# Kernel tuning notes

Hardware: AMD Instinct MI355X
Metric: run time of the kernel (lower is better)

The kernel has to match this reference:

```python
import jax, jax.numpy as jnp
import numpy as np

N_NODES = 50000
N_EDGES = 800000
NUM_FEAT = 256
HID = 64
N_CLS = 40
N_LAYERS = 2
EPS = 0.3  # residual scale from __init__ eps


def setup_inputs() -> dict:
    key = jax.random.key(0)
    ks = jax.random.split(key, 8)
    x = jax.random.normal(ks[0], (N_NODES, NUM_FEAT), dtype=jnp.float32)
    edge_index = jax.random.randint(ks[1], (2, N_EDGES), 0, N_NODES, dtype=jnp.int64)
    # xavier-normal-ish scaled weights
    W1 = jax.random.normal(ks[2], (HID, NUM_FEAT), dtype=jnp.float32) * (1.414 * (2.0 / (HID + NUM_FEAT)) ** 0.5)
    b1 = jnp.zeros((HID,), dtype=jnp.float32)
    W2 = jax.random.normal(ks[3], (N_CLS, HID), dtype=jnp.float32) * (1.414 * (2.0 / (N_CLS + HID)) ** 0.5)
    b2 = jnp.zeros((N_CLS,), dtype=jnp.float32)
    gate_w = jax.random.normal(ks[4], (N_LAYERS, 2 * HID), dtype=jnp.float32) * (1.414 * (2.0 / (2 * HID + 1)) ** 0.5)
    gate_b = jnp.zeros((N_LAYERS,), dtype=jnp.float32)
    return {"x": x, "edge_index": edge_index, "W1": W1, "b1": b1,
            "W2": W2, "b2": b2, "gate_w": gate_w, "gate_b": gate_b}


def _forward(x, edge_index, W1, b1, W2, b2, gate_w, gate_b):
    row, col = edge_index[0], edge_index[1]  # row = source, col = target (PyG convention)
    n = x.shape[0]
    ones_e = jnp.ones((edge_index.shape[1],), dtype=x.dtype)
    # degree(row) clamped to >=1, then d^{-1/2}
    deg = jnp.clip(jax.ops.segment_sum(ones_e, row, num_segments=n), 1.0)
    nd = deg ** -0.5  # [N]
    # mean-aggregation denominator: incoming-edge counts per target node
    cnt = jnp.clip(jax.ops.segment_sum(ones_e, col, num_segments=n), 1.0)

    # dense input projection (dropout is eval-mode no-op)
    h = jax.nn.relu(x @ W1.T + b1)  # [N, H]
    raw = h

    nd_edge = nd[row] * nd[col]  # [E]
    for l in range(N_LAYERS):
        hr = h[row]  # [E, H] gather (source)
        hc = h[col]  # [E, H] gather (target)
        # gate: Linear(concat([h[row], h[col]])) == h[row]@w_a + h[col]@w_b
        g = jnp.tanh(hr @ gate_w[l, :HID] + hc @ gate_w[l, HID:] + gate_b[l])  # [E]
        norm = g * nd_edge  # [E]
        msg = norm[:, None] * (hc + hr)  # x_i + x_j, [E, H]
        agg = jax.ops.segment_sum(msg, col, num_segments=n) / cnt[:, None]  # scatter-mean
        h = EPS * raw + agg

    logits = h @ W2.T + b2
    return jax.nn.log_softmax(logits, axis=1)


def reference(x, edge_index, W1, b1, W2, b2, gate_w, gate_b):
    return _forward(x, edge_index, W1, b1, W2, b2, gate_w, gate_b)
```

## Files before the change

### kernel.cpp

```cpp
#include <hip/hip_runtime.h>
#include <math.h>

#define N_NODES 50000
#define N_EDGES 800000
#define NFEAT 256
#define HID 64
#define NCLS 40
#define EPS_RES 0.3f
#define ROWSZ 68
#define SCAN_BLOCKS ((N_NODES + 255) / 256)
#define EB 32
#define CHUNK (N_EDGES / EB)
#define NR 4
#define RNG (N_NODES / NR)

typedef unsigned int uint;
typedef unsigned short ushort;

__device__ __forceinline__ float bflo(uint u) { return __uint_as_float(u << 16); }
__device__ __forceinline__ float bfhi(uint u) { return __uint_as_float(u & 0xFFFF0000u); }
__device__ __forceinline__ uint bf16rne(float f) {
    uint u = __float_as_uint(f);
    return (u + 0x7FFFu + ((u >> 16) & 1u)) >> 16;
}
__device__ __forceinline__ uint bf16rne2(float a, float b) {
    return bf16rne(a) | (bf16rne(b) << 16);
}

__global__ __launch_bounds__(256) void hist_kernel(const int* __restrict__ row,
                                                   const int* __restrict__ col,
                                                   int* __restrict__ degM,
                                                   int* __restrict__ cntM,
                                                   int* __restrict__ rank_local) {
    __shared__ int hist[RNG];
    int t = threadIdx.x;
    int chunk = blockIdx.x;
    int lo = blockIdx.y * RNG;
    int side = blockIdx.z;
    for (int j = t; j < RNG; j += 256) hist[j] = 0;
    __syncthreads();
    const int* idx = side ? col : row;
    int e0 = chunk * CHUNK;
    if (side == 0) {
        for (int base = 0; base < CHUNK; base += 1024) {
            int vb[4];
#pragma unroll
            for (int j = 0; j < 4; j++) {
                int i = base + j * 256 + t;
                vb[j] = (i < CHUNK) ? idx[e0 + i] : -1;
            }
#pragma unroll
            for (int j = 0; j < 4; j++) {
                uint v = (uint)(vb[j] - lo);
                if (v < RNG) atomicAdd(&hist[v], 1);
            }
        }
    } else {
        for (int base = 0; base < CHUNK; base += 1024) {
            int vb[4], ib[4];
#pragma unroll
            for (int j = 0; j < 4; j++) {
                int i = base + j * 256 + t;
                ib[j] = i;
                vb[j] = (i < CHUNK) ? idx[e0 + i] : -1;
            }
#pragma unroll
            for (int j = 0; j < 4; j++) {
                uint v = (uint)(vb[j] - lo);
                if (v < RNG) rank_local[e0 + ib[j]] = atomicAdd(&hist[v], 1);
            }
        }
    }
    __syncthreads();
    int* M = side ? cntM : degM;
    for (int j = t; j < RNG; j += 256) M[chunk * N_NODES + lo + j] = hist[j];
}

__device__ __forceinline__ int block_excl_scan_256(int v, int t, int* wsum) {
    int lane = t & 63, w = t >> 6;
    int sv = v;
#pragma unroll
    for (int d = 1; d < 64; d <<= 1) {
        int o = __shfl_up(sv, d);
        if (lane >= d) sv += o;
    }
    if (lane == 63) wsum[w] = sv;
    __syncthreads();
    int add = 0;
    for (int i = 0; i < w; i++) add += wsum[i];
    return sv + add - v;
}

__global__ void scan1_kernel(const int* __restrict__ degM, int* __restrict__ cntM,
                             int* __restrict__ off, int* __restrict__ bsum,
                             float* __restrict__ nd, float* __restrict__ invcnt) {
    __shared__ int wsum[4];
    int t = threadIdx.x;
    int idx = blockIdx.x * 256 + t;
    int v = 0;
    if (idx < N_NODES) {
        int sD = 0;
#pragma unroll
        for (int c = 0; c < EB; c++) sD += degM[c * N_NODES + idx];
        int run = 0;
#pragma unroll
        for (int c = 0; c < EB; c++) {
            int cv = cntM[c * N_NODES + idx];
            cntM[c * N_NODES + idx] = run;
            run += cv;
        }
        v = run;
        if (sD < 1) sD = 1;
        nd[idx] = rsqrtf((float)sD);
        int cc = run; if (cc < 1) cc = 1;
        invcnt[idx] = 1.0f / (float)cc;
    }
    int excl = block_excl_scan_256(v, t, wsum);
    if (idx < N_NODES) off[idx] = excl;
    if (t == 255) bsum[blockIdx.x] = excl + v;
}

__global__ void scan2_kernel(int* __restrict__ bsum) {
    __shared__ int wsum[4];
    int t = threadIdx.x;
    int v = (t < SCAN_BLOCKS) ? bsum[t] : 0;
    int excl = block_excl_scan_256(v, t, wsum);
    if (t < SCAN_BLOCKS) bsum[t] = excl;
}

__global__ void scan3_kernel(int* __restrict__ off, const int* __restrict__ bsum) {
    int t = threadIdx.x;
    int idx = blockIdx.x * 256 + t;
    if (idx < N_NODES) off[idx] += bsum[blockIdx.x];
    if (idx == 0) off[N_NODES] = N_EDGES;
}

__global__ void scatter_kernel(const int* __restrict__ row, const int* __restrict__ col,
                               const int* __restrict__ rank_local, const int* __restrict__ cntM,
                               const int* __restrict__ off, const float* __restrict__ nd,
                               int2* __restrict__ sedge) {
    int e = blockIdx.x * 256 + threadIdx.x;
    int r = row[e], c = col[e];
    int ch = e / CHUNK;
    int p = off[c] + cntM[ch * N_NODES + c] + rank_local[e];
    int2 se;
    se.x = r;
    se.y = __float_as_int(nd[r] * nd[c]);
    sedge[p] = se;
}

__global__ __launch_bounds__(256) void proj_kernel(const float* __restrict__ x,
                                                   const float* __restrict__ W1,
                                                   const float* __restrict__ b1,
                                                   const float* __restrict__ gw,
                                                   float* __restrict__ ha,
                                                   ushort* __restrict__ habf,
                                                   float* __restrict__ y,
                                                   float* __restrict__ z) {
    __shared__ float xs[64 * ROWSZ];
    __shared__ float ws[64 * ROWSZ];
    int t = threadIdx.x;
    int nb = blockIdx.x * 64;
    int lane = t & 63, w = t >> 6;
    int l15 = lane & 15, g = lane >> 4;
    int hbase = 16 * w + 4 * g;
    float acc[4][4];
#pragma unroll
    for (int j = 0; j < 4; j++)
#pragma unroll
        for (int i = 0; i < 4; i++) acc[j][i] = 0.f;

    for (int kc = 0; kc < NFEAT; kc += 64) {
        __syncthreads();
#pragma unroll
        for (int i = 0; i < 4; i++) {
            int idx = t + 256 * i;
            int r_ = idx >> 4;
            int kq = idx & 15;
            int gn = nb + r_;
            float4 v = make_float4(0.f, 0.f, 0.f, 0.f);
            if (gn < N_NODES) v = *(const float4*)(x + (size_t)gn * NFEAT + kc + kq * 4);
            *(float4*)(xs + r_ * ROWSZ + kq * 4) = v;
            float4 wv = *(const float4*)(W1 + (size_t)r_ * NFEAT + kc + kq * 4);
            *(float4*)(ws + r_ * ROWSZ + kq * 4) = wv;
        }
        __syncthreads();
#pragma unroll 4
        for (int k = 0; k < 64; k += 4) {
            float4 a[4], b[4];
#pragma unroll
            for (int j = 0; j < 4; j++) a[j] = *(const float4*)(xs + (l15 + 16 * j) * ROWSZ + k);
#pragma unroll
            for (int i = 0; i < 4; i++) b[i] = *(const float4*)(ws + (hbase + i) * ROWSZ + k);
#pragma unroll
            for (int j = 0; j < 4; j++)
#pragma unroll
                for (int i = 0; i < 4; i++)
                    acc[j][i] += a[j].x * b[i].x + a[j].y * b[i].y + a[j].z * b[i].z + a[j].w * b[i].w;
        }
    }
    float4 bias = *(const float4*)(b1 + hbase);
    float4 wa4 = *(const float4*)(gw + hbase);
    float4 wb4 = *(const float4*)(gw + HID + hbase);
    int slot = w * 4 + g;
    __syncthreads();
#pragma unroll
    for (int j = 0; j < 4; j++) {
        int gn = nb + l15 + 16 * j;
        float4 o;
        o.x = fmaxf(acc[j][0] + bias.x, 0.f);
        o.y = fmaxf(acc[j][1] + bias.y, 0.f);
        o.z = fmaxf(acc[j][2] + bias.z, 0.f);
        o.w = fmaxf(acc[j][3] + bias.w, 0.f);
        if (gn < N_NODES) {
            *(float4*)(ha + (size_t)gn * HID + hbase) = o;
            uint2 pk;
            pk.x = bf16rne2(o.x, o.y);
            pk.y = bf16rne2(o.z, o.w);
            *(uint2*)(habf + (size_t)gn * HID + hbase) = pk;
        }
        xs[(l15 + 16 * j) * 16 + slot] = o.x * wa4.x + o.y * wa4.y + o.z * wa4.z + o.w * wa4.w;
        ws[(l15 + 16 * j) * 16 + slot] = o.x * wb4.x + o.y * wb4.y + o.z * wb4.z + o.w * wb4.w;
    }
    __syncthreads();
    if (t < 64 && nb + t < N_NODES) {
        float sa = 0.f, sb = 0.f;
#pragma unroll
        for (int s = 0; s < 16; s++) { sa += xs[t * 16 + s]; sb += ws[t * 16 + s]; }
        y[nb + t] = sa;
        z[nb + t] = sb;
    }
}

__device__ __forceinline__ void agg_core8(const ushort* __restrict__ hbf,
                                          const int2* __restrict__ sedge,
                                          const float* __restrict__ y,
                                          float zc_b, int e0, int e1, int q, int c8,
                                          float acc[8], float& gs_out) {
#pragma unroll
    for (int i = 0; i < 8; i++) acc[i] = 0.f;
    float gs = 0.f;
    if (e0 < e1) {
        int eA = e0 + q;
        int ecA = (eA < e1) ? eA : e0;
        int2 seA = sedge[ecA];
        float ndeA = (eA < e1) ? __int_as_float(seA.y) : 0.f;
        int eB = e0 + 8 + q;
        int ecB = (eB < e1) ? eB : e0;
        int2 seB = sedge[ecB];
        float ndeB = (eB < e1) ? __int_as_float(seB.y) : 0.f;
        float yA = y[seA.x];
        uint4 uA = *(const uint4*)(hbf + (size_t)seA.x * HID + c8);
        for (int base = e0; base < e1; base += 8) {
            float yB = y[seB.x];
            uint4 uB = *(const uint4*)(hbf + (size_t)seB.x * HID + c8);
            int eC = base + 16 + q;
            int ecC = (eC < e1) ? eC : e0;
            int2 seC = sedge[ecC];
            float ndeC = (eC < e1) ? __int_as_float(seC.y) : 0.f;
            float gv = tanhf(yA + zc_b) * ndeA;
            acc[0] += gv * bflo(uA.x);
            acc[1] += gv * bfhi(uA.x);
            acc[2] += gv * bflo(uA.y);
            acc[3] += gv * bfhi(uA.y);
            acc[4] += gv * bflo(uA.z);
            acc[5] += gv * bfhi(uA.z);
            acc[6] += gv * bflo(uA.w);
            acc[7] += gv * bfhi(uA.w);
            gs += gv;
            yA = yB; uA = uB; ndeA = ndeB;
            seB = seC; ndeB = ndeC;
        }
    }
#pragma unroll
    for (int s = 8; s < 64; s <<= 1) {
#pragma unroll
        for (int i = 0; i < 8; i++) acc[i] += __shfl_xor(acc[i], s);
        gs += __shfl_xor(gs, s);
    }
    gs_out = gs;
}

__global__ void agg1_kernel(const float* __restrict__ ha, const ushort* __restrict__ habf,
                            const int2* __restrict__ sedge, const int* __restrict__ off,
                            const float* __restrict__ invcnt, const float* __restrict__ y,
                            const float* __restrict__ z, const float* __restrict__ gb,
                            const float* __restrict__ gw2, ushort* __restrict__ hbbf,
                            float* __restrict__ y2, float* __restrict__ z2) {
    int t = threadIdx.x;
    int lane = t & 63;
    int node = blockIdx.x * 4 + (t >> 6);
    int q = lane >> 3, c8 = (lane & 7) * 8;
    float4 ra = *(const float4*)(ha + (size_t)node * HID + c8);
    float4 rb = *(const float4*)(ha + (size_t)node * HID + c8 + 4);
    float raw8[8] = {ra.x, ra.y, ra.z, ra.w, rb.x, rb.y, rb.z, rb.w};
    float zc_b = z[node] + gb[0];
    float acc[8]; float gs;
    agg_core8(habf, sedge, y, zc_b, off[node], off[node + 1], q, c8, acc, gs);
    float invc = invcnt[node];
    float o[8];
#pragma unroll
    for (int i = 0; i < 8; i++) o[i] = EPS_RES * raw8[i] + (acc[i] + gs * raw8[i]) * invc;
    if (q == 0) {
        uint4 pk;
        pk.x = bf16rne2(o[0], o[1]);
        pk.y = bf16rne2(o[2], o[3]);
        pk.z = bf16rne2(o[4], o[5]);
        pk.w = bf16rne2(o[6], o[7]);
        *(uint4*)(hbbf + (size_t)node * HID + c8) = pk;
    }
    float4 wa0 = *(const float4*)(gw2 + c8);
    float4 wa1 = *(const float4*)(gw2 + c8 + 4);
    float4 wb0 = *(const float4*)(gw2 + HID + c8);
    float4 wb1 = *(const float4*)(gw2 + HID + c8 + 4);
    float p = o[0] * wa0.x + o[1] * wa0.y + o[2] * wa0.z + o[3] * wa0.w
            + o[4] * wa1.x + o[5] * wa1.y + o[6] * wa1.z + o[7] * wa1.w;
    float qq = o[0] * wb0.x + o[1] * wb0.y + o[2] * wb0.z + o[3] * wb0.w
             + o[4] * wb1.x + o[5] * wb1.y + o[6] * wb1.z + o[7] * wb1.w;
#pragma unroll
    for (int s = 1; s < 8; s <<= 1) { p += __shfl_xor(p, s); qq += __shfl_xor(qq, s); }
    if (lane == 0) { y2[node] = p; z2[node] = qq; }
}

__global__ void agg2_kernel(const ushort* __restrict__ hbbf, const float* __restrict__ ha,
                            const int2* __restrict__ sedge, const int* __restrict__ off,
                            const float* __restrict__ invcnt, const float* __restrict__ y2,
                            const float* __restrict__ z2, const float* __restrict__ gb,
                            const float* __restrict__ W2, const float* __restrict__ b2,
                            float* __restrict__ out) {
    __shared__ float w2s[NCLS * 65];
    __shared__ float b2s[NCLS];
    __shared__ float hs[4 * HID];
    int t = threadIdx.x;
    for (int i = t; i < NCLS * HID; i += 256) w2s[(i >> 6) * 65 + (i & 63)] = W2[i];
    if (t < NCLS) b2s[t] = b2[t];
    int lane = t & 63;
    int wv = t >> 6;
    int node = blockIdx.x * 4 + wv;
    int q = lane >> 3, c8 = (lane & 7) * 8;
    uint4 hc = *(const uint4*)(hbbf + (size_t)node * HID + c8);
    float hcv[8] = {bflo(hc.x), bfhi(hc.x), bflo(hc.y), bfhi(hc.y),
                    bflo(hc.z), bfhi(hc.z), bflo(hc.w), bfhi(hc.w)};
    float4 ra = *(const float4*)(ha + (size_t)node * HID + c8);
    float4 rb = *(const float4*)(ha + (size_t)node * HID + c8 + 4);
    float raw8[8] = {ra.x, ra.y, ra.z, ra.w, rb.x, rb.y, rb.z, rb.w};
    float zc_b = z2[node] + gb[0];
    float acc[8]; float gs;
    agg_core8(hbbf, sedge, y2, zc_b, off[node], off[node + 1], q, c8, acc, gs);
    float invc = invcnt[node];
    if (q == 0) {
        float4 o0, o1;
        o0.x = EPS_RES * raw8[0] + (acc[0] + gs * hcv[0]) * invc;
        o0.y = EPS_RES * raw8[1] + (acc[1] + gs * hcv[1]) * invc;
        o0.z = EPS_RES * raw8[2] + (acc[2] + gs * hcv[2]) * invc;
        o0.w = EPS_RES * raw8[3] + (acc[3] + gs * hcv[3]) * invc;
        o1.x = EPS_RES * raw8[4] + (acc[4] + gs * hcv[4]) * invc;
        o1.y = EPS_RES * raw8[5] + (acc[5] + gs * hcv[5]) * invc;
        o1.z = EPS_RES * raw8[6] + (acc[6] + gs * hcv[6]) * invc;
        o1.w = EPS_RES * raw8[7] + (acc[7] + gs * hcv[7]) * invc;
        *(float4*)(hs + wv * HID + c8) = o0;
        *(float4*)(hs + wv * HID + c8 + 4) = o1;
    }
    __syncthreads();
    float logit = 0.f;
    if (lane < NCLS) {
        const float* wr = w2s + lane * 65;
        const float* hrow = hs + wv * HID;
#pragma unroll
        for (int k = 0; k < HID; k++) logit += hrow[k] * wr[k];
        logit += b2s[lane];
    }
    float v = (lane < NCLS) ? logit : -INFINITY;
#pragma unroll
    for (int s = 1; s < 64; s <<= 1) v = fmaxf(v, __shfl_xor(v, s));
    float ex = (lane < NCLS) ? expf(logit - v) : 0.f;
#pragma unroll
    for (int s = 1; s < 64; s <<= 1) ex += __shfl_xor(ex, s);
    float ls = v + logf(ex);
    if (lane < NCLS) out[node * NCLS + lane] = logit - ls;
}

extern "C" void kernel_launch(void* const* d_in, const int* in_sizes, int n_in,
                              void* d_out, int out_size, void* d_ws, size_t ws_size,
                              hipStream_t stream) {
    const float* x  = (const float*)d_in[0];
    const int*   ei = (const int*)d_in[1];
    const float* W1 = (const float*)d_in[2];
    const float* b1 = (const float*)d_in[3];
    const float* W2 = (const float*)d_in[4];
    const float* b2 = (const float*)d_in[5];
    const float* gw = (const float*)d_in[6];
    const float* gb = (const float*)d_in[7];
    float* out = (float*)d_out;

    int2*  sedge  = (int2*)d_ws;
    float* nd     = (float*)(sedge + N_EDGES);
    float* invcnt = nd + N_NODES;
    float* y      = invcnt + N_NODES;
    float* z      = y + N_NODES;
    float* y2     = z + N_NODES;
    float* z2     = y2 + N_NODES;
    float* ha     = z2 + N_NODES;
    ushort* habf  = (ushort*)(ha + (size_t)N_NODES * HID);
    ushort* hbbf  = habf + (size_t)N_NODES * HID;
    int*   off    = (int*)(hbbf + (size_t)N_NODES * HID);
    int*   bsum   = off + N_NODES + 1;
    int*   degM   = (int*)ha;
    int*   cntM   = degM + (size_t)EB * N_NODES;
    int*   rank_local = (int*)habf;

    const int* row = ei;
    const int* col = ei + N_EDGES;

    hist_kernel<<<dim3(EB, NR, 2), 256, 0, stream>>>(row, col, degM, cntM, rank_local);
    scan1_kernel<<<SCAN_BLOCKS, 256, 0, stream>>>(degM, cntM, off, bsum, nd, invcnt);
    scan2_kernel<<<1, 256, 0, stream>>>(bsum);
    scan3_kernel<<<SCAN_BLOCKS, 256, 0, stream>>>(off, bsum);
    scatter_kernel<<<N_EDGES / 256, 256, 0, stream>>>(row, col, rank_local, cntM, off, nd, sedge);
    proj_kernel<<<(N_NODES + 63) / 64, 256, 0, stream>>>(x, W1, b1, gw, ha, habf, y, z);

    agg1_kernel<<<N_NODES / 4, 256, 0, stream>>>(ha, habf, sedge, off, invcnt, y, z, gb,
                                                 gw + 2 * HID, hbbf, y2, z2);
    agg2_kernel<<<N_NODES / 4, 256, 0, stream>>>(hbbf, ha, sedge, off, invcnt, y2, z2,
                                                 gb + 1, W2, b2, out);
}
```

Baseline: 268.1 us.

## Precompute per-edge gate weights in a separate kernel and drop the fp32 hidden copy

Adds a gate_kernel that computes tanh(y[src]+z[dst]+b) times the edge norm once per sorted edge. The scatter kernel now also writes a sorted target-column array for it to use. This removes the redundant per-lane tanh and y-gather from the aggregation inner loop, which now reads only a precomputed float per edge. The fp32 residual copy of h is also removed: both aggregation kernels read the residual from the bf16 buffer, which lowers precision. The cost is two extra edge-wide kernel launches and the writes and reads of an extra per-edge gate array.

Measured after the change: 285.0 us. 1.06x slower.

```diff
diff --git a/kernel.cpp b/kernel.cpp
--- a/kernel.cpp
+++ b/kernel.cpp
@@ -138,7 +138,7 @@
 __global__ void scatter_kernel(const int* __restrict__ row, const int* __restrict__ col,
                                const int* __restrict__ rank_local, const int* __restrict__ cntM,
                                const int* __restrict__ off, const float* __restrict__ nd,
-                               int2* __restrict__ sedge) {
+                               int2* __restrict__ sedge, int* __restrict__ scol) {
     int e = blockIdx.x * 256 + threadIdx.x;
     int r = row[e], c = col[e];
     int ch = e / CHUNK;
@@ -147,13 +147,13 @@
     se.x = r;
     se.y = __float_as_int(nd[r] * nd[c]);
     sedge[p] = se;
+    scol[p] = c;
 }
 
 __global__ __launch_bounds__(256) void proj_kernel(const float* __restrict__ x,
                                                    const float* __restrict__ W1,
                                                    const float* __restrict__ b1,
                                                    const float* __restrict__ gw,
-                                                   float* __restrict__ ha,
                                                    ushort* __restrict__ habf,
                                                    float* __restrict__ y,
                                                    float* __restrict__ z) {
@@ -213,7 +213,6 @@
         o.z = fmaxf(acc[j][2] + bias.z, 0.f);
         o.w = fmaxf(acc[j][3] + bias.w, 0.f);
         if (gn < N_NODES) {
-            *(float4*)(ha + (size_t)gn * HID + hbase) = o;
             uint2 pk;
             pk.x = bf16rne2(o.x, o.y);
             pk.y = bf16rne2(o.z, o.w);
@@ -232,10 +231,19 @@
     }
 }
 
+__global__ void gate_kernel(const int2* __restrict__ sedge, const int* __restrict__ scol,
+                            const float* __restrict__ y, const float* __restrict__ z,
+                            const float* __restrict__ gb, float* __restrict__ gnde) {
+    int e = blockIdx.x * 256 + threadIdx.x;
+    int2 se = sedge[e];
+    float g = tanhf(y[se.x] + z[scol[e]] + gb[0]);
+    gnde[e] = g * __int_as_float(se.y);
+}
+
 __device__ __forceinline__ void agg_core8(const ushort* __restrict__ hbf,
                                           const int2* __restrict__ sedge,
-                                          const float* __restrict__ y,
-                                          float zc_b, int e0, int e1, int q, int c8,
+                                          const float* __restrict__ gnde,
+                                          int e0, int e1, int q, int c8,
                                           float acc[8], float& gs_out) {
 #pragma unroll
     for (int i = 0; i < 8; i++) acc[i] = 0.f;
@@ -243,33 +251,30 @@
     if (e0 < e1) {
         int eA = e0 + q;
         int ecA = (eA < e1) ? eA : e0;
-        int2 seA = sedge[ecA];
-        float ndeA = (eA < e1) ? __int_as_float(seA.y) : 0.f;
+        int rA = sedge[ecA].x;
+        float gA = (eA < e1) ? gnde[ecA] : 0.f;
+        uint4 uA = *(const uint4*)(hbf + (size_t)rA * HID + c8);
         int eB = e0 + 8 + q;
         int ecB = (eB < e1) ? eB : e0;
-        int2 seB = sedge[ecB];
-        float ndeB = (eB < e1) ? __int_as_float(seB.y) : 0.f;
-        float yA = y[seA.x];
-        uint4 uA = *(const uint4*)(hbf + (size_t)seA.x * HID + c8);
+        int rB = sedge[ecB].x;
+        float gB = (eB < e1) ? gnde[ecB] : 0.f;
         for (int base = e0; base < e1; base += 8) {
-            float yB = y[seB.x];
-            uint4 uB = *(const uint4*)(hbf + (size_t)seB.x * HID + c8);
+            uint4 uB = *(const uint4*)(hbf + (size_t)rB * HID + c8);
             int eC = base + 16 + q;
             int ecC = (eC < e1) ? eC : e0;
-            int2 seC = sedge[ecC];
-            float ndeC = (eC < e1) ? __int_as_float(seC.y) : 0.f;
-            float gv = tanhf(yA + zc_b) * ndeA;
-            acc[0] += gv * bflo(uA.x);
-            acc[1] += gv * bfhi(uA.x);
-            acc[2] += gv * bflo(uA.y);
-            acc[3] += gv * bfhi(uA.y);
-            acc[4] += gv * bflo(uA.z);
-            acc[5] += gv * bfhi(uA.z);
-            acc[6] += gv * bflo(uA.w);
-            acc[7] += gv * bfhi(uA.w);
-            gs += gv;
-            yA = yB; uA = uB; ndeA = ndeB;
-            seB = seC; ndeB = ndeC;
+            int rC = sedge[ecC].x;
+            float gC = (eC < e1) ? gnde[ecC] : 0.f;
+            acc[0] += gA * bflo(uA.x);
+            acc[1] += gA * bfhi(uA.x);
+            acc[2] += gA * bflo(uA.y);
+            acc[3] += gA * bfhi(uA.y);
+            acc[4] += gA * bflo(uA.z);
+            acc[5] += gA * bfhi(uA.z);
+            acc[6] += gA * bflo(uA.w);
+            acc[7] += gA * bfhi(uA.w);
+            gs += gA;
+            uA = uB; gA = gB;
+            rB = rC; gB = gC;
         }
     }
 #pragma unroll
@@ -281,22 +286,20 @@
     gs_out = gs;
 }
 
-__global__ void agg1_kernel(const float* __restrict__ ha, const ushort* __restrict__ habf,
-                            const int2* __restrict__ sedge, const int* __restrict__ off,
-                            const float* __restrict__ invcnt, const float* __restrict__ y,
-                            const float* __restrict__ z, const float* __restrict__ gb,
-                            const float* __restrict__ gw2, ushort* __restrict__ hbbf,
-                            float* __restrict__ y2, float* __restrict__ z2) {
+__global__ void agg1_kernel(const ushort* __restrict__ habf, const int2* __restrict__ sedge,
+                            const float* __restrict__ gnde, const int* __restrict__ off,
+                            const float* __restrict__ invcnt, const float* __restrict__ gw2,
+                            ushort* __restrict__ hbbf, float* __restrict__ y2,
+                            float* __restrict__ z2) {
     int t = threadIdx.x;
     int lane = t & 63;
     int node = blockIdx.x * 4 + (t >> 6);
     int q = lane >> 3, c8 = (lane & 7) * 8;
-    float4 ra = *(const float4*)(ha + (size_t)node * HID + c8);
-    float4 rb = *(const float4*)(ha + (size_t)node * HID + c8 + 4);
-    float raw8[8] = {ra.x, ra.y, ra.z, ra.w, rb.x, rb.y, rb.z, rb.w};
-    float zc_b = z[node] + gb[0];
+    uint4 rw = *(const uint4*)(habf + (size_t)node * HID + c8);
+    float raw8[8] = {bflo(rw.x), bfhi(rw.x), bflo(rw.y), bfhi(rw.y),
+                     bflo(rw.z), bfhi(rw.z), bflo(rw.w), bfhi(rw.w)};
     float acc[8]; float gs;
-    agg_core8(habf, sedge, y, zc_b, off[node], off[node + 1], q, c8, acc, gs);
+    agg_core8(habf, sedge, gnde, off[node], off[node + 1], q, c8, acc, gs);
     float invc = invcnt[node];
     float o[8];
 #pragma unroll
@@ -322,10 +325,9 @@
     if (lane == 0) { y2[node] = p; z2[node] = qq; }
 }
 
-__global__ void agg2_kernel(const ushort* __restrict__ hbbf, const float* __restrict__ ha,
-                            const int2* __restrict__ sedge, const int* __restrict__ off,
-                            const float* __restrict__ invcnt, const float* __restrict__ y2,
-                            const float* __restrict__ z2, const float* __restrict__ gb,
+__global__ void agg2_kernel(const ushort* __restrict__ hbbf, const ushort* __restrict__ habf,
+                            const int2* __restrict__ sedge, const float* __restrict__ gnde,
+                            const int* __restrict__ off, const float* __restrict__ invcnt,
                             const float* __restrict__ W2, const float* __restrict__ b2,
                             float* __restrict__ out) {
     __shared__ float w2s[NCLS * 65];
@@ -341,12 +343,11 @@
     uint4 hc = *(const uint4*)(hbbf + (size_t)node * HID + c8);
     float hcv[8] = {bflo(hc.x), bfhi(hc.x), bflo(hc.y), bfhi(hc.y),
                     bflo(hc.z), bfhi(hc.z), bflo(hc.w), bfhi(hc.w)};
-    float4 ra = *(const float4*)(ha + (size_t)node * HID + c8);
-    float4 rb = *(const float4*)(ha + (size_t)node * HID + c8 + 4);
-    float raw8[8] = {ra.x, ra.y, ra.z, ra.w, rb.x, rb.y, rb.z, rb.w};
-    float zc_b = z2[node] + gb[0];
+    uint4 rw = *(const uint4*)(habf + (size_t)node * HID + c8);
+    float raw8[8] = {bflo(rw.x), bfhi(rw.x), bflo(rw.y), bfhi(rw.y),
+                     bflo(rw.z), bfhi(rw.z), bflo(rw.w), bfhi(rw.w)};
     float acc[8]; float gs;
-    agg_core8(hbbf, sedge, y2, zc_b, off[node], off[node + 1], q, c8, acc, gs);
+    agg_core8(hbbf, sedge, gnde, off[node], off[node + 1], q, c8, acc, gs);
     float invc = invcnt[node];
     if (q == 0) {
         float4 o0, o1;
@@ -394,20 +395,21 @@
     float* out = (float*)d_out;
 
     int2*  sedge  = (int2*)d_ws;
-    float* nd     = (float*)(sedge + N_EDGES);
+    int*   scol   = (int*)(sedge + N_EDGES);
+    float* gnde   = (float*)(scol + N_EDGES);
+    float* nd     = gnde + N_EDGES;
     float* invcnt = nd + N_NODES;
     float* y      = invcnt + N_NODES;
     float* z      = y + N_NODES;
     float* y2     = z + N_NODES;
     float* z2     = y2 + N_NODES;
-    float* ha     = z2 + N_NODES;
-    ushort* habf  = (ushort*)(ha + (size_t)N_NODES * HID);
+    ushort* habf  = (ushort*)(z2 + N_NODES);
     ushort* hbbf  = habf + (size_t)N_NODES * HID;
     int*   off    = (int*)(hbbf + (size_t)N_NODES * HID);
     int*   bsum   = off + N_NODES + 1;
-    int*   degM   = (int*)ha;
-    int*   cntM   = degM + (size_t)EB * N_NODES;
-    int*   rank_local = (int*)habf;
+    int*   degM   = (int*)habf;
+    int*   cntM   = (int*)hbbf;
+    int*   rank_local = (int*)gnde;
 
     const int* row = ei;
     const int* col = ei + N_EDGES;
@@ -416,11 +418,14 @@
     scan1_kernel<<<SCAN_BLOCKS, 256, 0, stream>>>(degM, cntM, off, bsum, nd, invcnt);
     scan2_kernel<<<1, 256, 0, stream>>>(bsum);
     scan3_kernel<<<SCAN_BLOCKS, 256, 0, stream>>>(off, bsum);
-    scatter_kernel<<<N_EDGES / 256, 256, 0, stream>>>(row, col, rank_local, cntM, off, nd, sedge);
-    proj_kernel<<<(N_NODES + 63) / 64, 256, 0, stream>>>(x, W1, b1, gw, ha, habf, y, z);
-
-    agg1_kernel<<<N_NODES / 4, 256, 0, stream>>>(ha, habf, sedge, off, invcnt, y, z, gb,
+    scatter_kernel<<<N_EDGES / 256, 256, 0, stream>>>(row, col, rank_local, cntM, off, nd,
+                                                      sedge, scol);
+    proj_kernel<<<(N_NODES + 63) / 64, 256, 0, stream>>>(x, W1, b1, gw, habf, y, z);
+
+    gate_kernel<<<N_EDGES / 256, 256, 0, stream>>>(sedge, scol, y, z, gb, gnde);
+    agg1_kernel<<<N_NODES / 4, 256, 0, stream>>>(habf, sedge, gnde, off, invcnt,
                                                  gw + 2 * HID, hbbf, y2, z2);
-    agg2_kernel<<<N_NODES / 4, 256, 0, stream>>>(hbbf, ha, sedge, off, invcnt, y2, z2,
-                                                 gb + 1, W2, b2, out);
-}
+    gate_kernel<<<N_EDGES / 256, 256, 0, stream>>>(sedge, scol, y2, z2, gb + 1, gnde);
+    agg2_kernel<<<N_NODES / 4, 256, 0, stream>>>(hbbf, habf, sedge, gnde, off, invcnt,
+                                                 W2, b2, out);
+}
```
